# Optimization experiments

Hardware: AMD Instinct MI355X
Metric: run time of the kernel (lower is better)

## Reference

```python
import jax, jax.numpy as jnp
import numpy as np

N = 50000
E = 800000
IN, HID, OUT, HEADS = 128, 64, 64, 3
NEG_SLOPE = 0.2
BN_EPS = 1e-5


def setup_inputs() -> dict:
    key = jax.random.key(0)
    ks = jax.random.split(key, 20)
    s = 0.05
    inp = {
        "x": jax.random.normal(ks[0], (N, IN), jnp.float32),
        "edge_index": jax.random.randint(ks[1], (2, E), 0, N, jnp.int32),
        # layer 0: in=128 -> heads=3, C=64 (concat -> 192)
        "Wl0": jax.random.normal(ks[2], (IN, HEADS * HID), jnp.float32) * s,
        "bl0": jnp.zeros((HEADS * HID,), jnp.float32),
        "Wr0": jax.random.normal(ks[3], (IN, HEADS * HID), jnp.float32) * s,
        "br0": jnp.zeros((HEADS * HID,), jnp.float32),
        "att0": jax.random.normal(ks[4], (HEADS, HID), jnp.float32) * s,
        "bias0": jnp.zeros((HEADS * HID,), jnp.float32),
        "gamma0": jnp.ones((HEADS * HID,), jnp.float32),
        "beta0": jnp.zeros((HEADS * HID,), jnp.float32),
        # layer 1: in=192 -> heads=1, C=64
        "Wl1": jax.random.normal(ks[5], (HEADS * HID, OUT), jnp.float32) * s,
        "bl1": jnp.zeros((OUT,), jnp.float32),
        "Wr1": jax.random.normal(ks[6], (HEADS * HID, OUT), jnp.float32) * s,
        "br1": jnp.zeros((OUT,), jnp.float32),
        "att1": jax.random.normal(ks[7], (1, OUT), jnp.float32) * s,
        "bias1": jnp.zeros((OUT,), jnp.float32),
        "gamma1": jnp.ones((OUT,), jnp.float32),
        "beta1": jnp.zeros((OUT,), jnp.float32),
    }
    return inp


def _gatv2_layer(x, Wl, bl, Wr, br, att, bias, src, dst, n):
    H, C = att.shape
    xl = (x @ Wl + bl).reshape(n, H, C)
    xr = (x @ Wr + br).reshape(n, H, C)
    e = jax.nn.leaky_relu(xl[src] + xr[dst], NEG_SLOPE)      # [E,H,C]
    logit = jnp.einsum("ehc,hc->eh", e, att)                 # [E,H]
    m = jax.lax.stop_gradient(jax.ops.segment_max(logit, dst, num_segments=n))
    p = jnp.exp(logit - m[dst])
    denom = jax.ops.segment_sum(p, dst, num_segments=n)
    alpha = p / denom[dst]                                   # per-dst softmax
    out = jax.ops.segment_sum(alpha[:, :, None] * xl[src], dst, num_segments=n)
    return out.reshape(n, H * C) + bias


def _bn(x, gamma, beta):
    mu = x.mean(0)
    var = x.var(0)
    return (x - mu) * jax.lax.rsqrt(var + BN_EPS) * gamma + beta


def reference(x, edge_index, Wl0, bl0, Wr0, br0, att0, bias0, gamma0, beta0,
              Wl1, bl1, Wr1, br1, att1, bias1, gamma1, beta1):
    n = x.shape[0]
    loops = jnp.arange(n, dtype=edge_index.dtype)
    src = jnp.concatenate([edge_index[0], loops])  # PyG add_self_loops=True
    dst = jnp.concatenate([edge_index[1], loops])
    h = _gatv2_layer(x, Wl0, bl0, Wr0, br0, att0, bias0, src, dst, n)
    h = _bn(jax.nn.relu(h), gamma0, beta0)
    h = _gatv2_layer(h, Wl1, bl1, Wr1, br1, att1, bias1, src, dst, n)
    h = _bn(jax.nn.relu(h), gamma1, beta1)
    return h
```

## Files before the change

### kernel.cpp

```cpp
#include <hip/hip_runtime.h>
#include <hip/hip_bf16.h>

#define LRELU_SLOPE 0.2f
#define BN_EPS 1e-5f

typedef __attribute__((ext_vector_type(8))) short short8v;
typedef __attribute__((ext_vector_type(4))) float float4v;

static __device__ __forceinline__ unsigned short f2bf(float f) {
    __hip_bfloat16 b = __float2bfloat16(f);
    return *reinterpret_cast<unsigned short*>(&b);
}
static __device__ __forceinline__ void unpack2(unsigned int u, float& f0, float& f1) {
    f0 = __uint_as_float(u << 16);
    f1 = __uint_as_float(u & 0xffff0000u);
}
static __device__ __forceinline__ float lrelu(float x) {
    return fmaxf(x, LRELU_SLOPE * x);
}

__global__ void convcount_kernel(const float* __restrict__ Wl0, const float* __restrict__ Wr0,
                                 const float* __restrict__ Wl1, const float* __restrict__ Wr1,
                                 unsigned short* __restrict__ Wt0, unsigned short* __restrict__ Wt1,
                                 const int* __restrict__ dst, int* __restrict__ counts, int E) {
    int idx = blockIdx.x * blockDim.x + threadIdx.x;
    if (idx < 384 * 128) {
        int c = idx >> 7, k = idx & 127;
        float v = (c < 192) ? Wl0[(size_t)k * 192 + c] : Wr0[(size_t)k * 192 + (c - 192)];
        Wt0[idx] = f2bf(v);
    } else if (idx < 384 * 128 + 128 * 192) {
        int i2 = idx - 384 * 128;
        int c = i2 / 192, k = i2 % 192;
        float v = (c < 64) ? Wl1[(size_t)k * 64 + c] : Wr1[(size_t)k * 64 + (c - 64)];
        Wt1[i2] = f2bf(v);
    }
    if (idx < E) atomicAdd(&counts[dst[idx]], 1);
}

__global__ void scanA_kernel(const int* __restrict__ counts, int* __restrict__ offs,
                             int* __restrict__ blkSum, int n) {
    __shared__ int wsum[4];
    const int lane = threadIdx.x & 63;
    const int wv = threadIdx.x >> 6;
    int i0 = blockIdx.x * 1024 + (int)threadIdx.x * 4;
    int v0 = (i0 + 0 < n) ? counts[i0 + 0] : 0;
    int v1 = (i0 + 1 < n) ? counts[i0 + 1] : 0;
    int v2 = (i0 + 2 < n) ? counts[i0 + 2] : 0;
    int v3 = (i0 + 3 < n) ? counts[i0 + 3] : 0;
    int s4 = v0 + v1 + v2 + v3;
    int s = s4;
    #pragma unroll
    for (int off = 1; off < 64; off <<= 1) {
        int t = __shfl_up(s, off, 64);
        if (lane >= off) s += t;
    }
    if (lane == 63) wsum[wv] = s;
    __syncthreads();
    int wpre = 0;
    for (int w = 0; w < wv; ++w) wpre += wsum[w];
    int excl = wpre + s - s4;
    if (i0 + 0 < n) offs[i0 + 0] = excl;
    excl += v0;
    if (i0 + 1 < n) offs[i0 + 1] = excl;
    excl += v1;
    if (i0 + 2 < n) offs[i0 + 2] = excl;
    excl += v2;
    if (i0 + 3 < n) offs[i0 + 3] = excl;
    if (threadIdx.x == 255) blkSum[blockIdx.x] = wpre + s;
}

__global__ void scanC_kernel(int* __restrict__ offs, const int* __restrict__ blkSum, int n, int E) {
    __shared__ int baseSh;
    const int b = blockIdx.x;
    if (threadIdx.x < 64) {
        int acc = 0;
        for (int i = threadIdx.x; i < b; i += 64) acc += blkSum[i];
        #pragma unroll
        for (int off = 1; off < 64; off <<= 1) acc += __shfl_xor(acc, off, 64);
        if (threadIdx.x == 0) baseSh = acc;
    }
    __syncthreads();
    const int base = baseSh;
    int i = b * 1024 + (int)threadIdx.x * 4;
    if (i + 3 < n) {
        int4 v = *reinterpret_cast<int4*>(&offs[i]);
        v.x += base; v.y += base; v.z += base; v.w += base;
        *reinterpret_cast<int4*>(&offs[i]) = v;
    } else {
        #pragma unroll
        for (int k = 0; k < 4; ++k)
            if (i + k < n) offs[i + k] += base;
    }
    if (b == 0 && threadIdx.x == 0) offs[n] = E;
}

__global__ void scatter_kernel(const int* __restrict__ src, const int* __restrict__ dst,
                               const int* __restrict__ offs, int* __restrict__ cursor,
                               int* __restrict__ esrc, int E) {
    int e = blockIdx.x * blockDim.x + threadIdx.x;
    if (e < E) {
        int d = dst[e];
        int pos = offs[d] + atomicAdd(&cursor[d], 1);
        esrc[pos] = src[e];
    }
}

template <int K, int NCH, bool BN>
__global__ __launch_bounds__(256) void mfma_dual_gemm(
    const float* __restrict__ X,
    const unsigned short* __restrict__ Wt,
    const float* __restrict__ bl, const float* __restrict__ br,
    const float* __restrict__ stats, const float* __restrict__ gamma,
    const float* __restrict__ beta, float invN,
    unsigned short* __restrict__ xlB, unsigned short* __restrict__ xrB, int N) {
    constexpr int LDA = 40;
    const int rowBase = blockIdx.x * 128;
    const int colBase = blockIdx.y * 128;

    __shared__ unsigned short SH[16896];
    unsigned short* XS = SH;
    unsigned short* WS = SH + 128 * LDA;
    __shared__ float ssA[K], ssB[K];

    const int tid = threadIdx.x;
    const int lane = tid & 63;
    const int wv = tid >> 6;
    const int lrow = lane & 15;
    const int lk = lane >> 4;

    if (BN) {
        for (int c = tid; c < K; c += 256) {
            float mu = stats[c] * invN;
            float var = stats[K + c] * invN - mu * mu;
            float sc = gamma[c] * rsqrtf(var + BN_EPS);
            ssA[c] = sc;
            ssB[c] = beta[c] - mu * sc;
        }
        __syncthreads();
    }

    float4v acc[2][8];
    #pragma unroll
    for (int i = 0; i < 2; ++i)
        #pragma unroll
        for (int j = 0; j < 8; ++j) acc[i][j] = (float4v){0.f, 0.f, 0.f, 0.f};

    for (int k0 = 0; k0 < K; k0 += 32) {
        {
            int r = tid >> 3;
            int kq = (tid & 7) * 4;
            float4 sc0, sc1;
            if (BN) {
                sc0 = *reinterpret_cast<const float4*>(&ssA[k0 + kq]);
                sc1 = *reinterpret_cast<const float4*>(&ssB[k0 + kq]);
            }
            #pragma unroll
            for (int i = 0; i < 4; ++i) {
                int row = r + 32 * i;
                int gr = rowBase + row;
                float4 v = make_float4(0.f, 0.f, 0.f, 0.f);
                if (gr < N) v = *reinterpret_cast<const float4*>(&X[(size_t)gr * K + k0 + kq]);
                if (BN) {
                    v.x = v.x * sc0.x + sc1.x;
                    v.y = v.y * sc0.y + sc1.y;
                    v.z = v.z * sc0.z + sc1.z;
                    v.w = v.w * sc0.w + sc1.w;
                }
                ushort4 u;
                u.x = f2bf(v.x); u.y = f2bf(v.y); u.z = f2bf(v.z); u.w = f2bf(v.w);
                *reinterpret_cast<ushort4*>(&XS[row * LDA + kq]) = u;
            }
        }
        {
            int c = tid >> 2;
            int kq8 = (tid & 3) * 8;
            #pragma unroll
            for (int i = 0; i < 2; ++i) {
                int col = c + 64 * i;
                uint4 w = *reinterpret_cast<const uint4*>(&Wt[(size_t)(colBase + col) * K + k0 + kq8]);
                *reinterpret_cast<uint4*>(&WS[col * LDA + kq8]) = w;
            }
        }
        __syncthreads();
        short8v aF[2], bF[8];
        #pragma unroll
        for (int rb = 0; rb < 2; ++rb)
            aF[rb] = *reinterpret_cast<const short8v*>(&XS[(wv * 32 + rb * 16 + lrow) * LDA + lk * 8]);
        #pragma unroll
        for (int cb = 0; cb < 8; ++cb)
            bF[cb] = *reinterpret_cast<const short8v*>(&WS[(cb * 16 + lrow) * LDA + lk * 8]);
        #pragma unroll
        for (int rb = 0; rb < 2; ++rb)
            #pragma unroll
            for (int cb = 0; cb < 8; ++cb)
                acc[rb][cb] = __builtin_amdgcn_mfma_f32_16x16x32_bf16(aF[rb], bF[cb], acc[rb][cb], 0, 0, 0);
        __syncthreads();
    }

    unsigned short* TR = SH + wv * (32 * 132);
    #pragma unroll
    for (int cb = 0; cb < 8; ++cb) {
        int cgG = colBase + cb * 16 + lrow;
        bool isR = cgG >= NCH;
        int cc = isR ? cgG - NCH : cgG;
        float bv = isR ? br[cc] : bl[cc];
        #pragma unroll
        for (int rb = 0; rb < 2; ++rb) {
            #pragma unroll
            for (int r = 0; r < 4; ++r) {
                int lr = rb * 16 + lk * 4 + r;
                TR[lr * 132 + cb * 16 + lrow] = f2bf(acc[rb][cb][r] + bv);
            }
        }
    }
    #pragma unroll
    for (int it = 0; it < 8; ++it) {
        int idx = it * 64 + lane;
        int lr = idx >> 4;
        int ck = (idx & 15) * 8;
        int grow = rowBase + wv * 32 + lr;
        if (grow < N) {
            uint4 v = *reinterpret_cast<const uint4*>(&TR[lr * 132 + ck]);
            int cgG = colBase + ck;
            bool isR = cgG >= NCH;
            int cc = isR ? cgG - NCH : cgG;
            int hh = cc >> 6;
            int ch = cc & 63;
            unsigned short* dstB = (isR ? xrB : xlB) + (size_t)hh * N * 64 + (size_t)grow * 64 + ch;
            *reinterpret_cast<uint4*>(dstB) = v;
        }
    }
}

template <int H>
__global__ __launch_bounds__(256) void gat_agg_head_kernel(
    const unsigned short* __restrict__ xlB,
    const unsigned short* __restrict__ xrB,
    const int* __restrict__ offs, const int* __restrict__ esrc,
    const float* __restrict__ att,
    const float* __restrict__ bias,
    float* __restrict__ outh,
    int N) {
    const int h = blockIdx.y;
    const unsigned short* xl_ = xlB + (size_t)h * N * 64;
    const unsigned short* xr_ = xrB + (size_t)h * N * 64;
    const int lane = threadIdx.x & 63;
    const int node = blockIdx.x * 4 + (threadIdx.x >> 6);
    if (node >= N) return;
    const int j = lane >> 3;
    const int cg = (lane & 7) * 8;

    float xr[8], at[8], acc[8];
    float den = 0.f;
    {
        uint4 u = *reinterpret_cast<const uint4*>(&xr_[(size_t)node * 64 + cg]);
        unpack2(u.x, xr[0], xr[1]); unpack2(u.y, xr[2], xr[3]);
        unpack2(u.z, xr[4], xr[5]); unpack2(u.w, xr[6], xr[7]);
        float4 a0 = *reinterpret_cast<const float4*>(&att[h * 64 + cg]);
        float4 a1 = *reinterpret_cast<const float4*>(&att[h * 64 + cg + 4]);
        at[0] = a0.x; at[1] = a0.y; at[2] = a0.z; at[3] = a0.w;
        at[4] = a1.x; at[5] = a1.y; at[6] = a1.z; at[7] = a1.w;
        #pragma unroll
        for (int c = 0; c < 8; ++c) acc[c] = 0.f;
    }

    const int beg = offs[node];
    const int total = offs[node + 1] - beg + 1;
    uint4 u0, u1;
    {
        int vc = (j < total) ? j : (total - 1);
        int s0 = (vc == 0) ? node : esrc[beg + vc - 1];
        u0 = *reinterpret_cast<const uint4*>(&xl_[(size_t)s0 * 64 + cg]);
        int v1i = j + 8;
        int vc1 = (v1i < total) ? v1i : (total - 1);
        int s1 = (vc1 == 0) ? node : esrc[beg + vc1 - 1];
        u1 = *reinterpret_cast<const uint4*>(&xl_[(size_t)s1 * 64 + cg]);
    }
    for (int t = 0; t < total; t += 8) {
        float xlv[8];
        unpack2(u0.x, xlv[0], xlv[1]); unpack2(u0.y, xlv[2], xlv[3]);
        unpack2(u0.z, xlv[4], xlv[5]); unpack2(u0.w, xlv[6], xlv[7]);
        u0 = u1;
        const int v2 = t + 16 + j;
        if (v2 < total) {
            int s2 = esrc[beg + v2 - 1];
            u1 = *reinterpret_cast<const uint4*>(&xl_[(size_t)s2 * 64 + cg]);
        }
        float s = 0.f;
        #pragma unroll
        for (int c = 0; c < 8; ++c) s += lrelu(xlv[c] + xr[c]) * at[c];
        #pragma unroll
        for (int off = 1; off <= 4; off <<= 1) s += __shfl_xor(s, off, 64);
        const float w = (t + j < total) ? 1.f : 0.f;
        float p = w * __expf(s);
        den += p;
        #pragma unroll
        for (int c = 0; c < 8; ++c) acc[c] += p * xlv[c];
    }

    #pragma unroll
    for (int off = 8; off <= 32; off <<= 1) {
        den += __shfl_xor(den, off, 64);
        #pragma unroll
        for (int c = 0; c < 8; ++c) acc[c] += __shfl_xor(acc[c], off, 64);
    }

    if (j == 0) {
        float inv = 1.f / den;
        float4 b0 = *reinterpret_cast<const float4*>(&bias[h * 64 + cg]);
        float4 b1 = *reinterpret_cast<const float4*>(&bias[h * 64 + cg + 4]);
        float4 o0, o1;
        o0.x = fmaxf(acc[0] * inv + b0.x, 0.f); o0.y = fmaxf(acc[1] * inv + b0.y, 0.f);
        o0.z = fmaxf(acc[2] * inv + b0.z, 0.f); o0.w = fmaxf(acc[3] * inv + b0.w, 0.f);
        o1.x = fmaxf(acc[4] * inv + b1.x, 0.f); o1.y = fmaxf(acc[5] * inv + b1.y, 0.f);
        o1.z = fmaxf(acc[6] * inv + b1.z, 0.f); o1.w = fmaxf(acc[7] * inv + b1.w, 0.f);
        float* orow = &outh[(size_t)node * (H * 64) + h * 64 + cg];
        *reinterpret_cast<float4*>(orow) = o0;
        *reinterpret_cast<float4*>(orow + 4) = o1;
    }
}

template <int CH>
__global__ void bn_stats_kernel(const float* __restrict__ h, float* __restrict__ stats, int N) {
    const int c = threadIdx.x;
    float s = 0.f, q = 0.f;
    for (int r = blockIdx.x; r < N; r += gridDim.x) {
        float v = h[(size_t)r * CH + c];
        s += v;
        q += v * v;
    }
    atomicAdd(&stats[c], s);
    atomicAdd(&stats[CH + c], q);
}

__global__ void bn_finapply64_kernel(float* __restrict__ h, const float* __restrict__ stats,
                                     const float* __restrict__ gamma, const float* __restrict__ beta,
                                     float invN, size_t total4) {
    size_t i = (size_t)blockIdx.x * blockDim.x + threadIdx.x;
    if (i >= total4) return;
    size_t e = i * 4;
    int c = (int)(e & 63);
    float4 v = *reinterpret_cast<float4*>(&h[e]);
    #pragma unroll
    for (int k = 0; k < 4; ++k) {
        float mu = stats[c + k] * invN;
        float var = stats[64 + c + k] * invN - mu * mu;
        float sc = gamma[c + k] * rsqrtf(var + BN_EPS);
        (&v.x)[k] = ((&v.x)[k] - mu) * sc + beta[c + k];
    }
    *reinterpret_cast<float4*>(&h[e]) = v;
}

extern "C" void kernel_launch(void* const* d_in, const int* in_sizes, int n_in,
                              void* d_out, int out_size, void* d_ws, size_t ws_size,
                              hipStream_t stream) {
    const float* x     = (const float*)d_in[0];
    const int*   eidx  = (const int*)d_in[1];
    const float* Wl0   = (const float*)d_in[2];
    const float* bl0   = (const float*)d_in[3];
    const float* Wr0   = (const float*)d_in[4];
    const float* br0   = (const float*)d_in[5];
    const float* att0  = (const float*)d_in[6];
    const float* bias0 = (const float*)d_in[7];
    const float* g0    = (const float*)d_in[8];
    const float* be0   = (const float*)d_in[9];
    const float* Wl1   = (const float*)d_in[10];
    const float* bl1   = (const float*)d_in[11];
    const float* Wr1   = (const float*)d_in[12];
    const float* br1   = (const float*)d_in[13];
    const float* att1  = (const float*)d_in[14];
    const float* bias1 = (const float*)d_in[15];
    const float* g1    = (const float*)d_in[16];
    const float* be1   = (const float*)d_in[17];

    const int N = in_sizes[0] / 128;
    const int E = in_sizes[1] / 2;
    const int* srcIdx = eidx;
    const int* dstIdx = eidx + E;
    const int nChunks = (N + 1023) >> 10;
    const int nGroups = (N + 3) / 4;
    const float invN = 1.f / (float)N;

    char* base = (char*)d_ws;
    auto alloc = [&](size_t bytes) {
        char* p = base;
        base += (bytes + 255) & ~(size_t)255;
        return p;
    };
    unsigned short* projL = (unsigned short*)alloc((size_t)3 * N * 64 * 2);
    unsigned short* projR = (unsigned short*)alloc((size_t)3 * N * 64 * 2);
    float* h0    = (float*)alloc((size_t)N * 192 * 4);
    int*   offs  = (int*)alloc((size_t)(N + 1) * 4);
    int*   esrc  = (int*)alloc((size_t)E * 4);
    int*   blkSum= (int*)alloc((size_t)nChunks * 4);
    unsigned short* Wt0 = (unsigned short*)alloc((size_t)384 * 128 * 2);
    unsigned short* Wt1 = (unsigned short*)alloc((size_t)128 * 192 * 2);
    char* zeroBeg = base;
    int*   counts = (int*)alloc((size_t)N * 4);
    int*   cursor = (int*)alloc((size_t)N * 4);
    float* stats0 = (float*)alloc(384 * 4);
    float* stats1 = (float*)alloc(128 * 4);
    size_t zeroBytes = (size_t)(base - zeroBeg);

    hipMemsetAsync(zeroBeg, 0, zeroBytes, stream);

    {
        int work = E > (384 * 128 + 128 * 192) ? E : (384 * 128 + 128 * 192);
        convcount_kernel<<<(work + 255) / 256, 256, 0, stream>>>(Wl0, Wr0, Wl1, Wr1, Wt0, Wt1, dstIdx, counts, E);
    }
    scanA_kernel<<<nChunks, 256, 0, stream>>>(counts, offs, blkSum, N);
    scanC_kernel<<<nChunks, 256, 0, stream>>>(offs, blkSum, N, E);
    scatter_kernel<<<(E + 255) / 256, 256, 0, stream>>>(srcIdx, dstIdx, offs, cursor, esrc, E);

    {
        dim3 grid((N + 127) / 128, 3);
        mfma_dual_gemm<128, 192, false><<<grid, 256, 0, stream>>>(
            x, Wt0, bl0, br0, nullptr, nullptr, nullptr, 0.f, projL, projR, N);
    }
    {
        dim3 grid(nGroups, 3);
        gat_agg_head_kernel<3><<<grid, 256, 0, stream>>>(projL, projR, offs, esrc, att0, bias0, h0, N);
    }
    bn_stats_kernel<192><<<256, 192, 0, stream>>>(h0, stats0, N);

    {
        dim3 grid((N + 127) / 128, 1);
        mfma_dual_gemm<192, 64, true><<<grid, 256, 0, stream>>>(
            h0, Wt1, bl1, br1, stats0, g0, be0, invN, projL, projR, N);
    }
    float* out = (float*)d_out;
    {
        dim3 grid(nGroups, 1);
        gat_agg_head_kernel<1><<<grid, 256, 0, stream>>>(projL, projR, offs, esrc, att1, bias1, out, N);
    }
    bn_stats_kernel<64><<<256, 64, 0, stream>>>(out, stats1, N);
    {
        size_t tot4 = (size_t)N * 16;
        bn_finapply64_kernel<<<(unsigned)((tot4 + 255) / 256), 256, 0, stream>>>(out, stats1, g1, be1, invN, tot4);
    }
}
```

Before: 363.9 us.

## Fuse CSR build into persistent kernel and fold BN stats into layer-1 aggregation

The four CSR-construction kernels (weight conversion plus degree count, two scan passes, scatter) become one persistent 256-block kernel that uses software grid barriers, which removes several launches. The layer-1 aggregation becomes a grid-stride kernel that accumulates BatchNorm sum and sum-of-squares in registers and LDS, so the separate stats pass over the output is dropped. The risks are that the spin-wait grid barrier deadlocks if all 256 blocks are not co-resident, and that the CSR phases now run on only 256 blocks.

```diff
diff --git a/kernel.cpp b/kernel.cpp
--- a/kernel.cpp
+++ b/kernel.cpp
@@ -19,86 +19,100 @@
     return fmaxf(x, LRELU_SLOPE * x);
 }
 
-__global__ void convcount_kernel(const float* __restrict__ Wl0, const float* __restrict__ Wr0,
-                                 const float* __restrict__ Wl1, const float* __restrict__ Wr1,
-                                 unsigned short* __restrict__ Wt0, unsigned short* __restrict__ Wt1,
-                                 const int* __restrict__ dst, int* __restrict__ counts, int E) {
-    int idx = blockIdx.x * blockDim.x + threadIdx.x;
-    if (idx < 384 * 128) {
-        int c = idx >> 7, k = idx & 127;
-        float v = (c < 192) ? Wl0[(size_t)k * 192 + c] : Wr0[(size_t)k * 192 + (c - 192)];
-        Wt0[idx] = f2bf(v);
-    } else if (idx < 384 * 128 + 128 * 192) {
-        int i2 = idx - 384 * 128;
-        int c = i2 / 192, k = i2 % 192;
-        float v = (c < 64) ? Wl1[(size_t)k * 64 + c] : Wr1[(size_t)k * 64 + (c - 64)];
-        Wt1[i2] = f2bf(v);
-    }
-    if (idx < E) atomicAdd(&counts[dst[idx]], 1);
-}
-
-__global__ void scanA_kernel(const int* __restrict__ counts, int* __restrict__ offs,
-                             int* __restrict__ blkSum, int n) {
+#define CSR_NB 256
+
+static __device__ __forceinline__ void gbar(unsigned* bar, unsigned target) {
+    __syncthreads();
+    if (threadIdx.x == 0) {
+        __threadfence();
+        atomicAdd(bar, 1u);
+        while (__hip_atomic_load(bar, __ATOMIC_RELAXED, __HIP_MEMORY_SCOPE_AGENT) < target)
+            __builtin_amdgcn_s_sleep(8);
+        __threadfence();
+    }
+    __syncthreads();
+}
+
+__global__ __launch_bounds__(256) void csr_all_kernel(
+    const float* __restrict__ Wl0, const float* __restrict__ Wr0,
+    const float* __restrict__ Wl1, const float* __restrict__ Wr1,
+    unsigned short* __restrict__ Wt0, unsigned short* __restrict__ Wt1,
+    const int* __restrict__ src, const int* __restrict__ dst,
+    int* __restrict__ counts, int* __restrict__ cursor,
+    int* __restrict__ offs, int* __restrict__ blkSum, int* __restrict__ esrc,
+    unsigned* __restrict__ bar,
+    int E, int N, int nChunks) {
+    const int gtid = blockIdx.x * 256 + threadIdx.x;
+    const int gstride = CSR_NB * 256;
+
+    for (int i = gtid; i < 384 * 128 + 128 * 192; i += gstride) {
+        if (i < 384 * 128) {
+            int c = i >> 7, k = i & 127;
+            float v = (c < 192) ? Wl0[(size_t)k * 192 + c] : Wr0[(size_t)k * 192 + (c - 192)];
+            Wt0[i] = f2bf(v);
+        } else {
+            int i2 = i - 384 * 128;
+            int c = i2 / 192, k = i2 % 192;
+            float v = (c < 64) ? Wl1[(size_t)k * 64 + c] : Wr1[(size_t)k * 64 + (c - 64)];
+            Wt1[i2] = f2bf(v);
+        }
+    }
+    for (int e = gtid; e < E; e += gstride) atomicAdd(&counts[dst[e]], 1);
+    gbar(bar, CSR_NB);
+
     __shared__ int wsum[4];
-    const int lane = threadIdx.x & 63;
-    const int wv = threadIdx.x >> 6;
-    int i0 = blockIdx.x * 1024 + (int)threadIdx.x * 4;
-    int v0 = (i0 + 0 < n) ? counts[i0 + 0] : 0;
-    int v1 = (i0 + 1 < n) ? counts[i0 + 1] : 0;
-    int v2 = (i0 + 2 < n) ? counts[i0 + 2] : 0;
-    int v3 = (i0 + 3 < n) ? counts[i0 + 3] : 0;
-    int s4 = v0 + v1 + v2 + v3;
-    int s = s4;
-    #pragma unroll
-    for (int off = 1; off < 64; off <<= 1) {
-        int t = __shfl_up(s, off, 64);
-        if (lane >= off) s += t;
-    }
-    if (lane == 63) wsum[wv] = s;
-    __syncthreads();
-    int wpre = 0;
-    for (int w = 0; w < wv; ++w) wpre += wsum[w];
-    int excl = wpre + s - s4;
-    if (i0 + 0 < n) offs[i0 + 0] = excl;
-    excl += v0;
-    if (i0 + 1 < n) offs[i0 + 1] = excl;
-    excl += v1;
-    if (i0 + 2 < n) offs[i0 + 2] = excl;
-    excl += v2;
-    if (i0 + 3 < n) offs[i0 + 3] = excl;
-    if (threadIdx.x == 255) blkSum[blockIdx.x] = wpre + s;
-}
-
-__global__ void scanC_kernel(int* __restrict__ offs, const int* __restrict__ blkSum, int n, int E) {
     __shared__ int baseSh;
-    const int b = blockIdx.x;
-    if (threadIdx.x < 64) {
-        int acc = 0;
-        for (int i = threadIdx.x; i < b; i += 64) acc += blkSum[i];
-        #pragma unroll
-        for (int off = 1; off < 64; off <<= 1) acc += __shfl_xor(acc, off, 64);
-        if (threadIdx.x == 0) baseSh = acc;
-    }
-    __syncthreads();
-    const int base = baseSh;
-    int i = b * 1024 + (int)threadIdx.x * 4;
-    if (i + 3 < n) {
-        int4 v = *reinterpret_cast<int4*>(&offs[i]);
-        v.x += base; v.y += base; v.z += base; v.w += base;
-        *reinterpret_cast<int4*>(&offs[i]) = v;
-    } else {
+    if ((int)blockIdx.x < nChunks) {
+        const int lane = threadIdx.x & 63;
+        const int wv = threadIdx.x >> 6;
+        int i0 = blockIdx.x * 1024 + (int)threadIdx.x * 4;
+        int v0 = (i0 + 0 < N) ? counts[i0 + 0] : 0;
+        int v1 = (i0 + 1 < N) ? counts[i0 + 1] : 0;
+        int v2 = (i0 + 2 < N) ? counts[i0 + 2] : 0;
+        int v3 = (i0 + 3 < N) ? counts[i0 + 3] : 0;
+        int s4 = v0 + v1 + v2 + v3;
+        int s = s4;
+        #pragma unroll
+        for (int off = 1; off < 64; off <<= 1) {
+            int t = __shfl_up(s, off, 64);
+            if (lane >= off) s += t;
+        }
+        if (lane == 63) wsum[wv] = s;
+        __syncthreads();
+        int wpre = 0;
+        for (int w = 0; w < wv; ++w) wpre += wsum[w];
+        int excl = wpre + s - s4;
+        if (i0 + 0 < N) offs[i0 + 0] = excl;
+        excl += v0;
+        if (i0 + 1 < N) offs[i0 + 1] = excl;
+        excl += v1;
+        if (i0 + 2 < N) offs[i0 + 2] = excl;
+        excl += v2;
+        if (i0 + 3 < N) offs[i0 + 3] = excl;
+        if (threadIdx.x == 255) blkSum[blockIdx.x] = wpre + s;
+    }
+    gbar(bar, 2 * CSR_NB);
+
+    if ((int)blockIdx.x < nChunks) {
+        const int b = blockIdx.x;
+        if (threadIdx.x < 64) {
+            int acc = 0;
+            for (int i = threadIdx.x; i < b; i += 64) acc += blkSum[i];
+            #pragma unroll
+            for (int off = 1; off < 64; off <<= 1) acc += __shfl_xor(acc, off, 64);
+            if (threadIdx.x == 0) baseSh = acc;
+        }
+        __syncthreads();
+        const int base = baseSh;
+        int i = b * 1024 + (int)threadIdx.x * 4;
         #pragma unroll
         for (int k = 0; k < 4; ++k)
-            if (i + k < n) offs[i + k] += base;
-    }
-    if (b == 0 && threadIdx.x == 0) offs[n] = E;
-}
-
-__global__ void scatter_kernel(const int* __restrict__ src, const int* __restrict__ dst,
-                               const int* __restrict__ offs, int* __restrict__ cursor,
-                               int* __restrict__ esrc, int E) {
-    int e = blockIdx.x * blockDim.x + threadIdx.x;
-    if (e < E) {
+            if (i + k < N) offs[i + k] += base;
+        if (b == 0 && threadIdx.x == 0) offs[N] = E;
+    }
+    gbar(bar, 3 * CSR_NB);
+
+    for (int e = gtid; e < E; e += gstride) {
         int d = dst[e];
         int pos = offs[d] + atomicAdd(&cursor[d], 1);
         esrc[pos] = src[e];
@@ -237,10 +251,8 @@
     const unsigned short* __restrict__ xlB,
     const unsigned short* __restrict__ xrB,
     const int* __restrict__ offs, const int* __restrict__ esrc,
-    const float* __restrict__ att,
-    const float* __restrict__ bias,
-    float* __restrict__ outh,
-    int N) {
+    const float* __restrict__ att, const float* __restrict__ bias,
+    float* __restrict__ outh, int N) {
     const int h = blockIdx.y;
     const unsigned short* xl_ = xlB + (size_t)h * N * 64;
     const unsigned short* xr_ = xrB + (size_t)h * N * 64;
@@ -318,6 +330,111 @@
         *reinterpret_cast<float4*>(orow) = o0;
         *reinterpret_cast<float4*>(orow + 4) = o1;
     }
+}
+
+__global__ __launch_bounds__(256) void gat_agg1_bn_kernel(
+    const unsigned short* __restrict__ xlB, const unsigned short* __restrict__ xrB,
+    const int* __restrict__ offs, const int* __restrict__ esrc,
+    const float* __restrict__ att, const float* __restrict__ bias,
+    float* __restrict__ outh, float* __restrict__ stats,
+    int N, int nGroups) {
+    __shared__ float ldsStats[128];
+    const int tid = threadIdx.x;
+    const int lane = tid & 63;
+    const int wv = tid >> 6;
+    const int j = lane >> 3;
+    const int cg = (lane & 7) * 8;
+
+    float at[8];
+    {
+        float4 a0 = *reinterpret_cast<const float4*>(&att[cg]);
+        float4 a1 = *reinterpret_cast<const float4*>(&att[cg + 4]);
+        at[0] = a0.x; at[1] = a0.y; at[2] = a0.z; at[3] = a0.w;
+        at[4] = a1.x; at[5] = a1.y; at[6] = a1.z; at[7] = a1.w;
+    }
+    float sSum[8] = {};
+    float sSq[8] = {};
+
+    for (int g = blockIdx.x; g < nGroups; g += gridDim.x) {
+        const int node = g * 4 + wv;
+        if (node >= N) continue;
+        float xr[8], acc[8];
+        float den = 0.f;
+        {
+            uint4 u = *reinterpret_cast<const uint4*>(&xrB[(size_t)node * 64 + cg]);
+            unpack2(u.x, xr[0], xr[1]); unpack2(u.y, xr[2], xr[3]);
+            unpack2(u.z, xr[4], xr[5]); unpack2(u.w, xr[6], xr[7]);
+            #pragma unroll
+            for (int c = 0; c < 8; ++c) acc[c] = 0.f;
+        }
+        const int beg = offs[node];
+        const int total = offs[node + 1] - beg + 1;
+        uint4 u0, u1;
+        {
+            int vc = (j < total) ? j : (total - 1);
+            int s0 = (vc == 0) ? node : esrc[beg + vc - 1];
+            u0 = *reinterpret_cast<const uint4*>(&xlB[(size_t)s0 * 64 + cg]);
+            int v1i = j + 8;
+            int vc1 = (v1i < total) ? v1i : (total - 1);
+            int s1 = (vc1 == 0) ? node : esrc[beg + vc1 - 1];
+            u1 = *reinterpret_cast<const uint4*>(&xlB[(size_t)s1 * 64 + cg]);
+        }
+        for (int t = 0; t < total; t += 8) {
+            float xlv[8];
+            unpack2(u0.x, xlv[0], xlv[1]); unpack2(u0.y, xlv[2], xlv[3]);
+            unpack2(u0.z, xlv[4], xlv[5]); unpack2(u0.w, xlv[6], xlv[7]);
+            u0 = u1;
+            const int v2 = t + 16 + j;
+            if (v2 < total) {
+                int s2 = esrc[beg + v2 - 1];
+                u1 = *reinterpret_cast<const uint4*>(&xlB[(size_t)s2 * 64 + cg]);
+            }
+            float s = 0.f;
+            #pragma unroll
+            for (int c = 0; c < 8; ++c) s += lrelu(xlv[c] + xr[c]) * at[c];
+            #pragma unroll
+            for (int off = 1; off <= 4; off <<= 1) s += __shfl_xor(s, off, 64);
+            const float w = (t + j < total) ? 1.f : 0.f;
+            float p = w * __expf(s);
+            den += p;
+            #pragma unroll
+            for (int c = 0; c < 8; ++c) acc[c] += p * xlv[c];
+        }
+        #pragma unroll
+        for (int off = 8; off <= 32; off <<= 1) {
+            den += __shfl_xor(den, off, 64);
+            #pragma unroll
+            for (int c = 0; c < 8; ++c) acc[c] += __shfl_xor(acc[c], off, 64);
+        }
+        if (j == 0) {
+            float inv = 1.f / den;
+            float4 b0 = *reinterpret_cast<const float4*>(&bias[cg]);
+            float4 b1 = *reinterpret_cast<const float4*>(&bias[cg + 4]);
+            float o[8];
+            o[0] = fmaxf(acc[0] * inv + b0.x, 0.f); o[1] = fmaxf(acc[1] * inv + b0.y, 0.f);
+            o[2] = fmaxf(acc[2] * inv + b0.z, 0.f); o[3] = fmaxf(acc[3] * inv + b0.w, 0.f);
+            o[4] = fmaxf(acc[4] * inv + b1.x, 0.f); o[5] = fmaxf(acc[5] * inv + b1.y, 0.f);
+            o[6] = fmaxf(acc[6] * inv + b1.z, 0.f); o[7] = fmaxf(acc[7] * inv + b1.w, 0.f);
+            *reinterpret_cast<float4*>(&outh[(size_t)node * 64 + cg]) = make_float4(o[0], o[1], o[2], o[3]);
+            *reinterpret_cast<float4*>(&outh[(size_t)node * 64 + cg + 4]) = make_float4(o[4], o[5], o[6], o[7]);
+            #pragma unroll
+            for (int c = 0; c < 8; ++c) {
+                sSum[c] += o[c];
+                sSq[c] += o[c] * o[c];
+            }
+        }
+    }
+    for (int i = tid; i < 128; i += 256) ldsStats[i] = 0.f;
+    __syncthreads();
+    if (j == 0) {
+        #pragma unroll
+        for (int c = 0; c < 8; ++c) {
+            atomicAdd(&ldsStats[cg + c], sSum[c]);
+            atomicAdd(&ldsStats[64 + cg + c], sSq[c]);
+        }
+    }
+    __syncthreads();
+    for (int i = tid; i < 128; i += 256) atomicAdd(&stats[i], ldsStats[i]);
 }
 
 template <int CH>
@@ -396,6 +513,7 @@
     unsigned short* Wt0 = (unsigned short*)alloc((size_t)384 * 128 * 2);
     unsigned short* Wt1 = (unsigned short*)alloc((size_t)128 * 192 * 2);
     char* zeroBeg = base;
+    unsigned* bar = (unsigned*)alloc(256);
     int*   counts = (int*)alloc((size_t)N * 4);
     int*   cursor = (int*)alloc((size_t)N * 4);
     float* stats0 = (float*)alloc(384 * 4);
@@ -404,23 +522,21 @@
 
     hipMemsetAsync(zeroBeg, 0, zeroBytes, stream);
 
-    {
-        int work = E > (384 * 128 + 128 * 192) ? E : (384 * 128 + 128 * 192);
-        convcount_kernel<<<(work + 255) / 256, 256, 0, stream>>>(Wl0, Wr0, Wl1, Wr1, Wt0, Wt1, dstIdx, counts, E);
-    }
-    scanA_kernel<<<nChunks, 256, 0, stream>>>(counts, offs, blkSum, N);
-    scanC_kernel<<<nChunks, 256, 0, stream>>>(offs, blkSum, N, E);
-    scatter_kernel<<<(E + 255) / 256, 256, 0, stream>>>(srcIdx, dstIdx, offs, cursor, esrc, E);
+    csr_all_kernel<<<CSR_NB, 256, 0, stream>>>(Wl0, Wr0, Wl1, Wr1, Wt0, Wt1,
+                                               srcIdx, dstIdx, counts, cursor,
+                                               offs, blkSum, esrc, bar, E, N, nChunks);
 
     {
         dim3 grid((N + 127) / 128, 3);
         mfma_dual_gemm<128, 192, false><<<grid, 256, 0, stream>>>(
             x, Wt0, bl0, br0, nullptr, nullptr, nullptr, 0.f, projL, projR, N);
     }
+
     {
         dim3 grid(nGroups, 3);
         gat_agg_head_kernel<3><<<grid, 256, 0, stream>>>(projL, projR, offs, esrc, att0, bias0, h0, N);
     }
+
     bn_stats_kernel<192><<<256, 192, 0, stream>>>(h0, stats0, N);
 
     {
@@ -428,12 +544,14 @@
         mfma_dual_gemm<192, 64, true><<<grid, 256, 0, stream>>>(
             h0, Wt1, bl1, br1, stats0, g0, be0, invN, projL, projR, N);
     }
+
     float* out = (float*)d_out;
     {
-        dim3 grid(nGroups, 1);
-        gat_agg_head_kernel<1><<<grid, 256, 0, stream>>>(projL, projR, offs, esrc, att1, bias1, out, N);
-    }
-    bn_stats_kernel<64><<<256, 64, 0, stream>>>(out, stats1, N);
+        int blocks = nGroups < 1024 ? nGroups : 1024;
+        gat_agg1_bn_kernel<<<blocks, 256, 0, stream>>>(projL, projR, offs, esrc, att1, bias1,
+                                                       out, stats1, N, nGroups);
+    }
+
     {
         size_t tot4 = (size_t)N * 16;
         bn_finapply64_kernel<<<(unsigned)((tot4 + 255) / 256), 256, 0, stream>>>(out, stats1, g1, be1, invN, tot4);
```

New measurement: 390.6 us. +7.4%, slower.
